# Kernel optimization log

Hardware: AMD Instinct MI355X
Metric: run time of the kernel (lower is better)

Reference implementation:

```python
import jax, jax.numpy as jnp
import numpy as np

NUM_HEADS = 16
HEAD_DIM = 64
ROPE_BASE = 160000.0


def _rope_tables(seq_len, head_dim):
    inv_freq = 1.0 / (ROPE_BASE ** (jnp.arange(0, head_dim, 2, dtype=jnp.float32) / head_dim))
    freqs = jnp.arange(seq_len, dtype=jnp.float32)[:, None] * inv_freq[None, :]  # [S, hd/2]
    return jnp.cos(freqs)[None, None], jnp.sin(freqs)[None, None]  # [1,1,S,hd/2]


def _apply_rope(x, cos, sin):
    # x: [B, nh, S, hd]; split-half rotation as in the torch module
    x1, x2 = jnp.split(x, 2, axis=-1)
    return jnp.concatenate([x1 * cos - x2 * sin, x2 * cos + x1 * sin], axis=-1)


def setup_inputs() -> dict:
    key = jax.random.key(0)
    k1, k2, k3 = jax.random.split(key, 3)
    B, S, H = 2, 2048, 1024
    hidden_states = jax.random.normal(k1, (B, S, H), dtype=jnp.float32)
    # additive causal mask: 0 for allowed, -1e9 for future positions
    causal = jnp.tril(jnp.ones((S, S), dtype=bool))
    attention_mask = jnp.where(causal, 0.0, -1e9).astype(jnp.float32)[None, None]
    Wqkv = jax.random.normal(k2, (H, 3 * H), dtype=jnp.float32) * (H ** -0.5)
    Wo = jax.random.normal(k3, (H, H), dtype=jnp.float32) * (H ** -0.5)
    return {"hidden_states": hidden_states, "attention_mask": attention_mask, "Wqkv": Wqkv, "Wo": Wo}


def reference(hidden_states, attention_mask, Wqkv, Wo):
    B, S, H = hidden_states.shape
    nh, hd = NUM_HEADS, HEAD_DIM
    scale = hd ** -0.5

    qkv = hidden_states @ Wqkv                                   # [B,S,3H]
    qkv = qkv.reshape(B, S, 3, nh, hd).transpose(2, 0, 3, 1, 4)  # [3,B,nh,S,hd]
    q, k, v = qkv[0], qkv[1], qkv[2]

    cos, sin = _rope_tables(S, hd)
    q = _apply_rope(q, cos, sin)
    k = _apply_rope(k, cos, sin)

    scores = jnp.einsum('bhqd,bhkd->bhqk', q, k) * scale + attention_mask
    attn = jax.nn.softmax(scores, axis=-1)
    out = jnp.einsum('bhqk,bhkd->bhqd', attn, v)                 # [B,nh,S,hd]
    out = out.transpose(0, 2, 1, 3).reshape(B, S, H)
    return out @ Wo
```

## Files before the change

### kernel.cpp

```cpp
#include <hip/hip_runtime.h>
#include <hip/hip_bf16.h>

typedef __bf16 bf16x8 __attribute__((ext_vector_type(8)));
typedef float f32x4 __attribute__((ext_vector_type(4)));
typedef unsigned short u16;

__device__ __forceinline__ u16 f2bf(float f) {
    union { float f; unsigned u; } x{f};
    unsigned r = x.u + 0x7fffu + ((x.u >> 16) & 1u);
    return (u16)(r >> 16);
}
__device__ __forceinline__ unsigned pk2(float a, float b) {
    union { float f; unsigned u; } x{a}, y{b};
    return ((x.u + 0x8000u) >> 16) | ((y.u + 0x8000u) & 0xffff0000u);
}
__device__ __forceinline__ float ex2(float x) { return __builtin_amdgcn_exp2f(x); }
__device__ __forceinline__ f32x4 zero4() { f32x4 z = {0.f, 0.f, 0.f, 0.f}; return z; }

typedef const __attribute__((address_space(1))) unsigned int* gp1_t;
typedef __attribute__((address_space(3))) unsigned int* lp3_t;
__device__ __forceinline__ void async16(const u16* g, u16* l) {
    __builtin_amdgcn_global_load_lds((gp1_t)g, (lp3_t)l, 16, 0, 0);
}

__global__ void __launch_bounds__(256) prep(const float* __restrict__ hs,
                                            u16* __restrict__ Xb,
                                            const float* __restrict__ Wqkv,
                                            u16* __restrict__ Wqkvt,
                                            const float* __restrict__ Wo,
                                            u16* __restrict__ Wot,
                                            float* __restrict__ cosT,
                                            float* __restrict__ sinT) {
    __shared__ float tile[32][33];
    const int blk = blockIdx.x, t = threadIdx.x;
    if (blk < 4096) {
        int i = (blk * 256 + t) * 4;
        float4 v = *(const float4*)(hs + i);
        ushort4 o;
        o.x = f2bf(v.x); o.y = f2bf(v.y); o.z = f2bf(v.z); o.w = f2bf(v.w);
        *(ushort4*)(Xb + i) = o;
    } else if (blk < 8192) {
        const float* W; u16* Wt; int N, bx, by;
        if (blk < 7168) { int bid = blk - 4096; W = Wqkv; Wt = Wqkvt; N = 3072; bx = bid % 96; by = bid / 96; }
        else            { int bid = blk - 7168; W = Wo;   Wt = Wot;   N = 1024; bx = bid % 32; by = bid / 32; }
        const int K = 1024;
        int tx = t & 31, ty = t >> 5;
        int n0 = bx * 32, k0 = by * 32;
#pragma unroll
        for (int i = 0; i < 32; i += 8)
            tile[ty + i][tx] = W[(size_t)(k0 + ty + i) * N + n0 + tx];
        __syncthreads();
#pragma unroll
        for (int i = 0; i < 32; i += 8)
            Wt[(size_t)(n0 + ty + i) * K + k0 + tx] = f2bf(tile[tx][ty + i]);
    } else {
        int idx = (blk - 8192) * 256 + t;
        int d = idx & 31, s = idx >> 5;
        float inv = expf(-(float)d * 0.374466538f);
        float th = (float)s * inv;
        cosT[idx] = cosf(th);
        sinT[idx] = sinf(th);
    }
}

struct GemmCtx {
    f32x4 acc[4][4];
    int m16, q4, wm, wn;
};
template <int KDIM>
__device__ __forceinline__ void gemm_loop(const u16* __restrict__ A,
                                          const u16* __restrict__ Bt,
                                          int bm, int bn, GemmCtx& cx,
                                          u16* As, u16* Bs) {
    const int t = threadIdx.x;
    const int lane = t & 63, w = t >> 6;
    cx.wm = w >> 1; cx.wn = w & 1;
    cx.m16 = lane & 15; cx.q4 = lane >> 4;

    const int lrow = lane >> 2;
    const int kchunk = (lane & 3) ^ ((lane >> 3) & 3);
    const u16* Ag = A + (size_t)(bm * 128 + w * 32 + lrow) * KDIM + kchunk * 8;
    const u16* Bg = Bt + (size_t)(bn * 128 + w * 32 + lrow) * KDIM + kchunk * 8;
    u16* Al0 = As + (w * 32) * 32;
    u16* Al1 = As + (w * 32 + 16) * 32;
    u16* Bl0 = Bs + (w * 32) * 32;
    u16* Bl1 = Bs + (w * 32 + 16) * 32;
    const int kswz = (cx.q4 ^ ((cx.m16 >> 1) & 3)) * 8;

#pragma unroll
    for (int i = 0; i < 4; i++)
#pragma unroll
        for (int j = 0; j < 4; j++) cx.acc[i][j] = zero4();

    for (int k0 = 0; k0 < KDIM; k0 += 32) {
        __syncthreads();
        async16(Ag + k0, Al0);
        async16(Ag + 16 * KDIM + k0, Al1);
        async16(Bg + k0, Bl0);
        async16(Bg + 16 * KDIM + k0, Bl1);
        __syncthreads();
        bf16x8 af[4], bf[4];
#pragma unroll
        for (int i = 0; i < 4; i++)
            af[i] = *(const bf16x8*)&As[(cx.wm * 64 + i * 16 + cx.m16) * 32 + kswz];
#pragma unroll
        for (int j = 0; j < 4; j++)
            bf[j] = *(const bf16x8*)&Bs[(cx.wn * 64 + j * 16 + cx.m16) * 32 + kswz];
#pragma unroll
        for (int i = 0; i < 4; i++)
#pragma unroll
            for (int j = 0; j < 4; j++)
                cx.acc[i][j] = __builtin_amdgcn_mfma_f32_16x16x32_bf16(af[i], bf[j], cx.acc[i][j], 0, 0, 0);
    }
}

__global__ void __launch_bounds__(256) gemm_qkv(const u16* __restrict__ A,
                                                const u16* __restrict__ Bt,
                                                const float* __restrict__ cosT,
                                                const float* __restrict__ sinT,
                                                u16* __restrict__ Q,
                                                u16* __restrict__ Kd,
                                                u16* __restrict__ Vt) {
    __shared__ __align__(16) u16 As[128 * 32];
    __shared__ __align__(16) u16 Bs[128 * 32];
    GemmCtx cx;
    const int bm = blockIdx.y, bn = blockIdx.x;
    gemm_loop<1024>(A, Bt, bm, bn, cx, As, Bs);
    const int m16 = cx.m16, q4 = cx.q4;

    const int colbase = bn * 128 + cx.wn * 64;
    const int type = colbase >> 10;
    const int h = (colbase & 1023) >> 6;
    const int rbase = bm * 128 + cx.wm * 64;

    if (type == 2) {
#pragma unroll
        for (int i = 0; i < 4; i++) {
            int s0 = rbase + i * 16 + q4 * 4;
            int b = s0 >> 11, sl = s0 & 2047;
            size_t ob = (size_t)(b * 16 + h) * 64 * 2048;
#pragma unroll
            for (int j = 0; j < 4; j++) {
                int d = j * 16 + m16;
                ushort4 o;
                o.x = f2bf(cx.acc[i][j][0]);
                o.y = f2bf(cx.acc[i][j][1]);
                o.z = f2bf(cx.acc[i][j][2]);
                o.w = f2bf(cx.acc[i][j][3]);
                *(ushort4*)&Vt[ob + (size_t)d * 2048 + sl] = o;
            }
        }
    } else {
        u16* dst = (type == 0) ? Q : Kd;
        const float qs = (type == 0) ? 0.1803368801f  : 1.0f;
#pragma unroll
        for (int i = 0; i < 4; i++)
#pragma unroll
            for (int rr = 0; rr < 4; rr++) {
                int r = rbase + i * 16 + q4 * 4 + rr;
                int b = r >> 11, s = r & 2047;
                size_t ob = ((size_t)((b * 16 + h) * 2048 + s)) * 64;
#pragma unroll
                for (int j2 = 0; j2 < 2; j2++) {
                    int d = j2 * 16 + m16;
                    float cs = cosT[s * 32 + d];
                    float sn = sinT[s * 32 + d];
                    float x1 = cx.acc[i][j2][rr];
                    float x2 = cx.acc[i][j2 + 2][rr];
                    dst[ob + d]      = f2bf((x1 * cs - x2 * sn) * qs);
                    dst[ob + d + 32] = f2bf((x2 * cs + x1 * sn) * qs);
                }
            }
    }
}

__global__ void __launch_bounds__(256) gemm_out(const u16* __restrict__ A,
                                                const u16* __restrict__ Bt,
                                                float* __restrict__ C) {
    __shared__ __align__(16) u16 As[128 * 32];
    __shared__ __align__(16) u16 Bs[128 * 32];
    GemmCtx cx;
    const int bm = blockIdx.y, bn = blockIdx.x;
    gemm_loop<1024>(A, Bt, bm, bn, cx, As, Bs);
    const int N = 1024;
#pragma unroll
    for (int i = 0; i < 4; i++)
#pragma unroll
        for (int j = 0; j < 4; j++)
#pragma unroll
            for (int rr = 0; rr < 4; rr++) {
                int row = bm * 128 + cx.wm * 64 + i * 16 + cx.q4 * 4 + rr;
                int col = bn * 128 + cx.wn * 64 + j * 16 + cx.m16;
                C[(size_t)row * N + col] = cx.acc[i][j][rr];
            }
}

__global__ void __launch_bounds__(512) attn_kernel(const u16* __restrict__ Q,
                                                   const u16* __restrict__ Kg_,
                                                   const u16* __restrict__ Vtg_,
                                                   u16* __restrict__ O) {
    __shared__ __align__(16) u16 Ks[2][64][72];
    __shared__ __align__(16) u16 Vs[2][64][72];
    __shared__ __align__(16) u16 Pt[8][16][72];
    const int t = threadIdx.x, w = t >> 6;
    const int m16 = t & 15, q4 = (t & 63) >> 4;
    const int bx = blockIdx.x, bh = blockIdx.y;
    const size_t base = (size_t)bh * 2048 * 64;
    const int b = bh >> 4, h = bh & 15;
    const int skey = t >> 3, sc = (t & 7) * 8;

#pragma unroll 1
    for (int ph = 0; ph < 2; ph++) {
        const int st = ph ? (15 - bx) : bx;
        const int qrow = st * 128 + w * 16 + m16;
        const u16* Qg = Q + base + (size_t)qrow * 64;
        bf16x8 qf0 = *(const bf16x8*)(Qg + q4 * 8);
        bf16x8 qf1 = *(const bf16x8*)(Qg + 32 + q4 * 8);

        f32x4 occ[4];
#pragma unroll
        for (int dc = 0; dc < 4; dc++) occ[dc] = zero4();
        float li = 0.f;

        const int jtmax = 2 * st + 1;
        const int jd = 2 * st + (w >> 2);

        const u16* Kb0 = Kg_ + base + skey * 64 + sc;
        const u16* Vt0 = Vtg_ + base + (size_t)skey * 2048 + sc;
        uint4 ka = *(const uint4*)(Kb0);
        uint4 va = *(const uint4*)(Vt0);

#pragma unroll 1
        for (int jt = 0; jt <= jtmax; jt++) {
            const int bi = jt & 1;
            *(uint4*)&Ks[bi][skey][sc] = ka;
            *(uint4*)&Vs[bi][skey][sc] = va;
            if (jt < jtmax) {
                ka = *(const uint4*)(Kb0 + (size_t)(jt + 1) * 4096);
                va = *(const uint4*)(Vt0 + (size_t)(jt + 1) * 64);
            }
            __syncthreads();

            if (jt <= jd) {
                f32x4 stv[4];
#pragma unroll
                for (int c = 0; c < 4; c++) stv[c] = zero4();
#pragma unroll
                for (int c = 0; c < 4; c++) {
                    bf16x8 kf0 = *(const bf16x8*)&Ks[bi][c * 16 + m16][q4 * 8];
                    bf16x8 kf1 = *(const bf16x8*)&Ks[bi][c * 16 + m16][32 + q4 * 8];
                    stv[c] = __builtin_amdgcn_mfma_f32_16x16x32_bf16(kf0, qf0, stv[c], 0, 0, 0);
                    stv[c] = __builtin_amdgcn_mfma_f32_16x16x32_bf16(kf1, qf1, stv[c], 0, 0, 0);
                }

                float pv[4][4];
#pragma unroll
                for (int c = 0; c < 4; c++)
#pragma unroll
                    for (int rr = 0; rr < 4; rr++) pv[c][rr] = stv[c][rr];
                if (jt == jd) {
                    const int ql = qrow - 64 * jt;
#pragma unroll
                    for (int c = 0; c < 4; c++)
#pragma unroll
                        for (int rr = 0; rr < 4; rr++)
                            if (c * 16 + q4 * 4 + rr > ql) pv[c][rr] = -1e30f;
                }

#pragma unroll
                for (int c = 0; c < 4; c++) {
                    float p0 = ex2(pv[c][0] - 24.f);
                    float p1 = ex2(pv[c][1] - 24.f);
                    float p2 = ex2(pv[c][2] - 24.f);
                    float p3 = ex2(pv[c][3] - 24.f);
                    li += (p0 + p1) + (p2 + p3);
                    *(uint2*)&Pt[w][m16][c * 16 + q4 * 4] = make_uint2(pk2(p0, p1), pk2(p2, p3));
                }

#pragma unroll
                for (int ks = 0; ks < 2; ks++) {
                    bf16x8 pf = *(const bf16x8*)&Pt[w][m16][ks * 32 + q4 * 8];
#pragma unroll
                    for (int dc = 0; dc < 4; dc++) {
                        bf16x8 vf = *(const bf16x8*)&Vs[bi][dc * 16 + m16][ks * 32 + q4 * 8];
                        occ[dc] = __builtin_amdgcn_mfma_f32_16x16x32_bf16(vf, pf, occ[dc], 0, 0, 0);
                    }
                }
            }
        }

        li += __shfl_xor(li, 16);
        li += __shfl_xor(li, 32);
        float rli = 1.0f / li;
        u16* Op = O + ((size_t)(b * 2048 + qrow)) * 1024 + h * 64 + q4 * 4;
#pragma unroll
        for (int dc = 0; dc < 4; dc++) {
            ushort4 o;
            o.x = f2bf(occ[dc][0] * rli);
            o.y = f2bf(occ[dc][1] * rli);
            o.z = f2bf(occ[dc][2] * rli);
            o.w = f2bf(occ[dc][3] * rli);
            *(ushort4*)(Op + dc * 16) = o;
        }
        __syncthreads();
    }
}

extern "C" void kernel_launch(void* const* d_in, const int* in_sizes, int n_in,
                              void* d_out, int out_size, void* d_ws, size_t ws_size,
                              hipStream_t stream) {
    const float* hs   = (const float*)d_in[0];
    const float* Wqkv = (const float*)d_in[2];
    const float* Wo   = (const float*)d_in[3];
    float* out = (float*)d_out;

    const int BS = 4096;
    const int H = 1024, N3 = 3072;
    const int SH = 32 * 2048 * 64;

    u16* Xb    = (u16*)d_ws;
    u16* Wqkvt = Xb + (size_t)BS * H;
    u16* Wot   = Wqkvt + (size_t)N3 * H;
    u16* Qb    = Wot + (size_t)H * H;
    u16* Kb    = Qb + SH;
    u16* Vtb   = Kb + SH;
    u16* AOb   = Vtb + SH;
    float* cosT = (float*)(AOb + (size_t)BS * H);
    float* sinT = cosT + 2048 * 32;

    prep<<<8448, 256, 0, stream>>>(hs, Xb, Wqkv, Wqkvt, Wo, Wot, cosT, sinT);

    gemm_qkv<<<dim3(N3 / 128, BS / 128), 256, 0, stream>>>(Xb, Wqkvt, cosT, sinT,
                                                           Qb, Kb, Vtb);

    attn_kernel<<<dim3(8, 32), 512, 0, stream>>>(Qb, Kb, Vtb, AOb);

    gemm_out<<<dim3(H / 128, BS / 128), 256, 0, stream>>>(AOb, Wot, out);
}
```

Baseline: 199.7 us.

## Double-buffer LDS tiles in GEMM loop to overlap global loads with MFMA

Turns the GEMM main loop into a two-stage software pipeline. The next k-tile is fetched into a second LDS buffer with async global_load_lds while MFMAs run on the current one, and explicit vmcnt waits plus s_barrier replace the two __syncthreads per iteration. This hides global-load latency behind compute. In exchange, LDS per block doubles, which may reduce occupancy, and the hand-placed waitcnt and barrier logic is fragile.

```diff
diff --git a/kernel.cpp b/kernel.cpp
--- a/kernel.cpp
+++ b/kernel.cpp
@@ -81,10 +81,8 @@
     const int kchunk = (lane & 3) ^ ((lane >> 3) & 3);
     const u16* Ag = A + (size_t)(bm * 128 + w * 32 + lrow) * KDIM + kchunk * 8;
     const u16* Bg = Bt + (size_t)(bn * 128 + w * 32 + lrow) * KDIM + kchunk * 8;
-    u16* Al0 = As + (w * 32) * 32;
-    u16* Al1 = As + (w * 32 + 16) * 32;
-    u16* Bl0 = Bs + (w * 32) * 32;
-    u16* Bl1 = Bs + (w * 32 + 16) * 32;
+    const int l0 = (w * 32) * 32;
+    const int l1 = (w * 32 + 16) * 32;
     const int kswz = (cx.q4 ^ ((cx.m16 >> 1) & 3)) * 8;
 
 #pragma unroll
@@ -92,25 +90,46 @@
 #pragma unroll
         for (int j = 0; j < 4; j++) cx.acc[i][j] = zero4();
 
-    for (int k0 = 0; k0 < KDIM; k0 += 32) {
-        __syncthreads();
-        async16(Ag + k0, Al0);
-        async16(Ag + 16 * KDIM + k0, Al1);
-        async16(Bg + k0, Bl0);
-        async16(Bg + 16 * KDIM + k0, Bl1);
-        __syncthreads();
+    constexpr int NT = KDIM / 32;
+    async16(Ag, As + l0);
+    async16(Ag + 16 * KDIM, As + l1);
+    async16(Bg, Bs + l0);
+    async16(Bg + 16 * KDIM, Bs + l1);
+
+#pragma unroll 1
+    for (int tt = 0; tt < NT; ++tt) {
+        const int co = (tt & 1) * 4096;
+        if (tt + 1 < NT) {
+            const int no = 4096 - co;
+            const int k0 = (tt + 1) * 32;
+            async16(Ag + k0, As + no + l0);
+            async16(Ag + 16 * KDIM + k0, As + no + l1);
+            async16(Bg + k0, Bs + no + l0);
+            async16(Bg + 16 * KDIM + k0, Bs + no + l1);
+            asm volatile("s_waitcnt vmcnt(4)" ::: "memory");
+        } else {
+            asm volatile("s_waitcnt vmcnt(0)" ::: "memory");
+        }
+        __builtin_amdgcn_s_barrier();
+        asm volatile("" ::: "memory");
+        __builtin_amdgcn_sched_barrier(0);
+
         bf16x8 af[4], bf[4];
 #pragma unroll
         for (int i = 0; i < 4; i++)
-            af[i] = *(const bf16x8*)&As[(cx.wm * 64 + i * 16 + cx.m16) * 32 + kswz];
+            af[i] = *(const bf16x8*)&As[co + (cx.wm * 64 + i * 16 + cx.m16) * 32 + kswz];
 #pragma unroll
         for (int j = 0; j < 4; j++)
-            bf[j] = *(const bf16x8*)&Bs[(cx.wn * 64 + j * 16 + cx.m16) * 32 + kswz];
+            bf[j] = *(const bf16x8*)&Bs[co + (cx.wn * 64 + j * 16 + cx.m16) * 32 + kswz];
 #pragma unroll
         for (int i = 0; i < 4; i++)
 #pragma unroll
             for (int j = 0; j < 4; j++)
                 cx.acc[i][j] = __builtin_amdgcn_mfma_f32_16x16x32_bf16(af[i], bf[j], cx.acc[i][j], 0, 0, 0);
+
+        asm volatile("" ::: "memory");
+        __builtin_amdgcn_sched_barrier(0);
+        __builtin_amdgcn_s_barrier();
     }
 }
 
@@ -121,8 +140,8 @@
                                                 u16* __restrict__ Q,
                                                 u16* __restrict__ Kd,
                                                 u16* __restrict__ Vt) {
-    __shared__ __align__(16) u16 As[128 * 32];
-    __shared__ __align__(16) u16 Bs[128 * 32];
+    __shared__ __align__(16) u16 As[2 * 128 * 32];
+    __shared__ __align__(16) u16 Bs[2 * 128 * 32];
     GemmCtx cx;
     const int bm = blockIdx.y, bn = blockIdx.x;
     gemm_loop<1024>(A, Bt, bm, bn, cx, As, Bs);
@@ -177,8 +196,8 @@
 __global__ void __launch_bounds__(256) gemm_out(const u16* __restrict__ A,
                                                 const u16* __restrict__ Bt,
                                                 float* __restrict__ C) {
-    __shared__ __align__(16) u16 As[128 * 32];
-    __shared__ __align__(16) u16 Bs[128 * 32];
+    __shared__ __align__(16) u16 As[2 * 128 * 32];
+    __shared__ __align__(16) u16 Bs[2 * 128 * 32];
     GemmCtx cx;
     const int bm = blockIdx.y, bn = blockIdx.x;
     gemm_loop<1024>(A, Bt, bm, bn, cx, As, Bs);
```

Result: no change. 200.9 us (+0.6%).
